# Kernel optimization log

Hardware: AMD Instinct MI355X
Metric: run time of the kernel (lower is better)

Reference implementation:

```python
import jax, jax.numpy as jnp
import numpy as np

D = 128       # embedding_dim
BC = 64       # block_count
BS = 512      # block_size
K = 6         # main conv kernel size
OV = 2 * BC   # overlap_size
SCALE = 1.0 / np.sqrt(D).astype(np.float32)


def setup_inputs() -> dict:
    key = jax.random.key(0)
    ks = jax.random.split(key, 6)
    B = 8
    x = jax.random.normal(ks[0], (B, BC * BS, D), dtype=jnp.float32)
    w_lw = jax.random.normal(ks[1], (D, 1), dtype=jnp.float32) * 0.05
    b_lw = jnp.zeros((1,), dtype=jnp.float32)
    conv_w = jax.random.normal(ks[2], (D, D, K), dtype=jnp.float32) * 0.05  # (out, in, k)
    conv_b = jnp.zeros((D,), dtype=jnp.float32)
    fusion_w = jax.random.normal(ks[3], (3 * D, D), dtype=jnp.float32) * 0.05
    fusion_b = jnp.zeros((D,), dtype=jnp.float32)
    return {"x": x, "w_lw": w_lw, "b_lw": b_lw, "conv_w": conv_w,
            "conv_b": conv_b, "fusion_w": fusion_w, "fusion_b": fusion_b}


def _prefix_softmax_weighted_sum(x, logits):
    # x: (B, L, D), logits: (B, L) -- faithful replica of the torch scan
    pmax = jax.lax.cummax(logits, axis=1)
    ex = jnp.exp(logits - pmax)                    # (B, L)
    psum = jnp.cumsum(ex, axis=1)                  # (B, L)
    wpre = jnp.cumsum(ex[..., None] * x, axis=1)   # (B, L, D)
    return wpre / psum[..., None]


def _attn(q, k, v):
    # q: (N, 1, D); k, v: (N, S, D)
    s = jnp.einsum('nqd,nkd->nqk', q, k) * SCALE
    return jnp.einsum('nqk,nkd->nqd', jax.nn.softmax(s, axis=-1), v)


def reference(x, w_lw, b_lw, conv_w, conv_b, fusion_w, fusion_b):
    B, L, _ = x.shape  # L == BC * BS, so F.pad in the original is a no-op
    logits = jax.nn.silu(x @ w_lw + b_lw)[..., 0]          # (B, L)
    prefix_x = _prefix_softmax_weighted_sum(x, logits) + x  # (B, L, D)

    # per-block conv1d (kernel 6, padding='same' in torch => pad (2,3))
    blocks = prefix_x.reshape(B * BC, BS, D).transpose(0, 2, 1)  # (N, D, BS)
    conv = jax.lax.conv_general_dilated(
        blocks, conv_w, window_strides=(1,), padding=[(2, 3)],
        dimension_numbers=('NCH', 'OIH', 'NCH')) + conv_b[None, :, None]
    blocks_c = conv.transpose(0, 2, 1)                           # (N, BS, D)
    block_repr = jnp.max(blocks_c, axis=1)[:, None, :]           # (N, 1, D)

    # overlap windows: replicate-pad end by OV//2, slice, gather OV-wide windows
    xov = jnp.pad(prefix_x, ((0, 0), (0, OV // 2), (0, 0)), mode='edge')
    xov = xov[:, BS - OV // 2:, :]                               # (B, (BC-1)*BS + OV, D)
    idx = (jnp.arange(BC) * BS)[:, None] + jnp.arange(OV)[None, :]  # (BC, OV)
    xbo = xov[:, idx, :].reshape(B * BC, OV, D)

    a_s = _attn(block_repr, blocks_c, blocks_c)  # block->self
    a_o = _attn(block_repr, xbo, xbo)            # block->overlap
    fused = jnp.concatenate([a_s, a_o, block_repr], axis=-1)    # (N, 1, 3D)
    out = (fused @ fusion_w + fusion_b).reshape(B, BC, D)
    return (out, out)
```

## Files before the change

kernel.cpp:

```cpp
#include <hip/hip_runtime.h>
#include <hip/hip_bf16.h>

#define NB 8
#define LSEQ 32768
#define DCH 128
#define NCHUNK 1024
#define NSUB 4096
#define NBLK 512
#define PH 520
#define SCALE_F 0.08838834764831845f

typedef __bf16 bf16x8 __attribute__((ext_vector_type(8)));
typedef float f32x4 __attribute__((ext_vector_type(4)));

__device__ __forceinline__ float bf2f(unsigned short u) {
    return __uint_as_float(((unsigned)u) << 16);
}
__device__ __forceinline__ unsigned short f2bf(float f) {
    unsigned u = __float_as_uint(f);
    u += 0x7fffu + ((u >> 16) & 1u);
    return (unsigned short)(u >> 16);
}

__device__ __forceinline__ void async_copy16(const void* gsrc, void* ldst) {
    __builtin_amdgcn_global_load_lds(
        (const __attribute__((address_space(1))) unsigned int*)gsrc,
        (__attribute__((address_space(3))) unsigned int*)ldst, 16, 0, 0);
}

__global__ __launch_bounds__(256) void k_logits2(const float* __restrict__ x,
                                                 const float* __restrict__ w_lw,
                                                 const float* __restrict__ b_lw,
                                                 float* __restrict__ logits,
                                                 float* __restrict__ subM) {
    int chunk = blockIdx.x, t = threadIdx.x;
    int g = t & 15, rs = t >> 4;
    __shared__ float sp[256 * 17];
    __shared__ float red[256];
    float wv[8];
    #pragma unroll
    for (int e = 0; e < 8; ++e) wv[e] = w_lw[g * 8 + e];
    float bb = b_lw[0];
    size_t base = (size_t)chunk * 256 * DCH;
    for (int i = 0; i < 16; ++i) {
        int row = rs * 16 + i;
        float4 a  = *(const float4*)(x + base + (size_t)row * DCH + g * 8);
        float4 b4 = *(const float4*)(x + base + (size_t)row * DCH + g * 8 + 4);
        sp[row * 17 + g] = a.x * wv[0] + a.y * wv[1] + a.z * wv[2] + a.w * wv[3] +
                           b4.x * wv[4] + b4.y * wv[5] + b4.z * wv[6] + b4.w * wv[7];
    }
    __syncthreads();
    float s = bb;
    #pragma unroll
    for (int j = 0; j < 16; ++j) s += sp[t * 17 + j];
    float l = s / (1.f + expf(-s));
    logits[(size_t)chunk * 256 + t] = l;
    red[t] = l;
    __syncthreads();
    for (int off = 32; off >= 1; off >>= 1) {
        if ((t & 63) < off) red[t] = fmaxf(red[t], red[t + off]);
        __syncthreads();
    }
    if ((t & 63) == 0) subM[chunk * 4 + (t >> 6)] = red[t];
}

__global__ __launch_bounds__(64) void k_seed_max2(const float* __restrict__ subM,
                                                  float* __restrict__ seedM) {
    int b = blockIdx.x, lane = threadIdx.x;
    const float* src = subM + b * 512;
    float* dst = seedM + b * 512;
    float v[8];
    float m = -INFINITY;
    #pragma unroll
    for (int j = 0; j < 8; ++j) { v[j] = src[lane * 8 + j]; m = fmaxf(m, v[j]); }
    float incl = m;
    #pragma unroll
    for (int off = 1; off < 64; off <<= 1) {
        float o = __shfl_up(incl, off, 64);
        if (lane >= off) incl = fmaxf(incl, o);
    }
    float ex = __shfl_up(incl, 1, 64);
    if (lane == 0) ex = -INFINITY;
    float run = ex;
    #pragma unroll
    for (int j = 0; j < 8; ++j) { dst[lane * 8 + j] = run; run = fmaxf(run, v[j]); }
}

__global__ __launch_bounds__(256) void k_sums(const float* __restrict__ x,
                                              const float* __restrict__ logits,
                                              const float* __restrict__ seedM,
                                              float* __restrict__ exg,
                                              float* __restrict__ S_w,
                                              float* __restrict__ S_wx) {
    int chunk = blockIdx.x, t = threadIdx.x;
    int g = t & 15, rs = t >> 4;
    __shared__ float llog[256];
    __shared__ float wbuf[256];
    __shared__ float red[256];
    __shared__ float rp[16 * 130];
    llog[t] = logits[(size_t)chunk * 256 + t];
    __syncthreads();
    if (t < 4) {
        float M = seedM[chunk * 4 + t];
        float m = -INFINITY;
        for (int i = 0; i < 64; ++i) {
            float l = llog[t * 64 + i];
            m = fmaxf(m, l);
            wbuf[t * 64 + i] = expf(l - fmaxf(M, m));
        }
    }
    __syncthreads();
    float w_t = wbuf[t];
    exg[(size_t)chunk * 256 + t] = w_t;
    red[t] = w_t;
    __syncthreads();
    for (int off = 32; off >= 1; off >>= 1) {
        if ((t & 63) < off) red[t] += red[t + off];
        __syncthreads();
    }
    if ((t & 63) == 0) S_w[chunk * 4 + (t >> 6)] = red[t];
    float acc[8];
    #pragma unroll
    for (int e = 0; e < 8; ++e) acc[e] = 0.f;
    size_t base = (size_t)chunk * 256 * DCH;
    for (int i = 0; i < 16; ++i) {
        int row = rs * 16 + i;
        float w = wbuf[row];
        float4 a  = *(const float4*)(x + base + (size_t)row * DCH + g * 8);
        float4 b4 = *(const float4*)(x + base + (size_t)row * DCH + g * 8 + 4);
        acc[0] += w * a.x;  acc[1] += w * a.y;  acc[2] += w * a.z;  acc[3] += w * a.w;
        acc[4] += w * b4.x; acc[5] += w * b4.y; acc[6] += w * b4.z; acc[7] += w * b4.w;
    }
    #pragma unroll
    for (int e = 0; e < 8; ++e) rp[rs * 130 + g * 8 + e] = acc[e];
    __syncthreads();
    #pragma unroll
    for (int k = 0; k < 2; ++k) {
        int idx = k * 256 + t;
        int sub = idx >> 7, c = idx & 127;
        float sm = rp[(sub * 4 + 0) * 130 + c] + rp[(sub * 4 + 1) * 130 + c] +
                   rp[(sub * 4 + 2) * 130 + c] + rp[(sub * 4 + 3) * 130 + c];
        S_wx[((size_t)chunk * 4 + sub) * DCH + c] = sm;
    }
}

__global__ __launch_bounds__(64) void k_seed_w(const float* __restrict__ S_w,
                                               float* __restrict__ sS_w) {
    int b = blockIdx.x, lane = threadIdx.x;
    const float* src = S_w + b * 512;
    float* dst = sS_w + b * 512;
    float v[8];
    float tot = 0.f;
    #pragma unroll
    for (int j = 0; j < 8; ++j) { v[j] = src[lane * 8 + j]; tot += v[j]; }
    float incl = tot;
    #pragma unroll
    for (int off = 1; off < 64; off <<= 1) {
        float o = __shfl_up(incl, off, 64);
        if (lane >= off) incl += o;
    }
    float ex = __shfl_up(incl, 1, 64);
    if (lane == 0) ex = 0.f;
    float run = ex;
    #pragma unroll
    for (int j = 0; j < 8; ++j) { dst[lane * 8 + j] = run; run += v[j]; }
}

__global__ __launch_bounds__(256) void k_seed_sums2(const float* __restrict__ S_wx,
                                                    float* __restrict__ sS_wx) {
    int b = blockIdx.x >> 3, cg = blockIdx.x & 7;
    int t = threadIdx.x;
    int cl = t & 15, seg = t >> 4;
    int c = cg * 16 + cl;
    __shared__ float tots[16][17];
    const float* src = S_wx + (size_t)b * 512 * DCH + c;
    float* dst = sS_wx + (size_t)b * 512 * DCH + c;
    int s0 = seg * 32;
    float tot = 0.f;
    for (int j = 0; j < 32; ++j) tot += src[(size_t)(s0 + j) * DCH];
    tots[seg][cl] = tot;
    __syncthreads();
    if (t < 16) {
        float run = 0.f;
        for (int s = 0; s < 16; ++s) { float tmp = tots[s][t]; tots[s][t] = run; run += tmp; }
    }
    __syncthreads();
    float run = tots[seg][cl];
    for (int j = 0; j < 32; ++j) {
        float val = src[(size_t)(s0 + j) * DCH];
        dst[(size_t)(s0 + j) * DCH] = run;
        run += val;
    }
}

__global__ __launch_bounds__(256) void k_zero_pad(unsigned short* __restrict__ P) {
    int n = blockIdx.x, t = threadIdx.x;
    for (int i = t; i < 1024; i += 256) {
        int rr = i >> 7;
        int row = (rr < 2) ? rr : 512 + rr;
        P[(n * PH + row) * DCH + (i & 127)] = 0;
    }
}

__global__ __launch_bounds__(128) void k_apply(const float* __restrict__ x,
                                               const float* __restrict__ exg,
                                               const float* __restrict__ sS_w,
                                               const float* __restrict__ sS_wx,
                                               unsigned short* __restrict__ P) {
    int t = threadIdx.x, w = t >> 6, lane = t & 63;
    int s = blockIdx.x * 2 + w;
    int b = s >> 9, sb = s & 511;
    __shared__ float e2[128];
    e2[t] = exg[(size_t)blockIdx.x * 128 + t];
    float2 axx = *(const float2*)(sS_wx + (size_t)s * DCH + 2 * lane);
    float aex = sS_w[s];
    __syncthreads();
    const float* es = e2 + w * 64;
    int pib0 = sb * 64;
    int n = b * 64 + (pib0 >> 9);
    int row0 = (pib0 & 511) + 2;
    const float* xp = x + ((size_t)b * LSEQ + pib0) * DCH + 2 * lane;
    unsigned short* pp = P + ((size_t)n * PH + row0) * DCH + 2 * lane;
    for (int j = 0; j < 64; ++j) {
        float e = es[j];
        aex += e;
        float2 xv = *(const float2*)xp;
        axx.x += e * xv.x;
        axx.y += e * xv.y;
        float inv = 1.f / aex;
        unsigned pk = ((unsigned)f2bf(axx.y * inv + xv.y) << 16) | f2bf(axx.x * inv + xv.x);
        *(unsigned*)pp = pk;
        xp += DCH;
        pp += DCH;
    }
}

__global__ __launch_bounds__(256) void k_w2t(const float* __restrict__ conv_w,
                                             unsigned short* __restrict__ W2t) {
    int idx = blockIdx.x * 256 + threadIdx.x;
    if (idx < 128 * 768) {
        int o = idx / 768, kk = idx % 768;
        int kn = kk >> 7, i = kk & 127;
        W2t[idx] = f2bf(conv_w[(o * 128 + i) * 6 + kn]);
    }
}

__global__ __launch_bounds__(256) void k_conv(const unsigned short* __restrict__ P,
                                              const unsigned short* __restrict__ W2t,
                                              const float* __restrict__ conv_b,
                                              unsigned short* __restrict__ convout) {
    int n = blockIdx.x >> 2;
    int h0 = (blockIdx.x & 3) * 128;
    __shared__ __align__(16) unsigned short lds[128 * 136];
    char* ldsA = (char*)lds;
    char* ldsB = (char*)lds + 16384;
    int t = threadIdx.x;
    int wave = t >> 6, lane = t & 63;
    f32x4 acc[4][4] = {};
    const unsigned short* Pn = P + (size_t)n * PH * DCH;
    int wm = (wave >> 1) * 64, wn = (wave & 1) * 64;
    int rdma = (lane >> 3);
    int cpos = lane & 7;

    for (int kt = 0; kt < 12; ++kt) {
        int kn = kt >> 1;
        int c0 = (kt & 1) * 64;
        __syncthreads();
        #pragma unroll
        for (int j = 0; j < 4; ++j) {
            int r = (wave * 4 + j) * 8 + rdma;
            int gr = h0 + kn + r;
            int csrcA = cpos ^ (gr & 7);
            async_copy16(Pn + (size_t)gr * DCH + c0 + csrcA * 8,
                         ldsA + (wave * 4 + j) * 1024 + lane * 16);
            int csrcB = cpos ^ (r & 7);
            async_copy16(W2t + (size_t)r * 768 + kt * 64 + csrcB * 8,
                         ldsB + (wave * 4 + j) * 1024 + lane * 16);
        }
        __syncthreads();
        #pragma unroll
        for (int ks = 0; ks < 2; ++ks) {
            bf16x8 af[4], bfr[4];
            #pragma unroll
            for (int mi = 0; mi < 4; ++mi) {
                int rA = wm + mi * 16 + (lane & 15);
                int pA = (ks * 4 + (lane >> 4)) ^ ((kn + rA) & 7);
                af[mi] = *(const bf16x8*)(ldsA + rA * 128 + pA * 16);
            }
            #pragma unroll
            for (int ni = 0; ni < 4; ++ni) {
                int oB = wn + ni * 16 + (lane & 15);
                int pB = (ks * 4 + (lane >> 4)) ^ (oB & 7);
                bfr[ni] = *(const bf16x8*)(ldsB + oB * 128 + pB * 16);
            }
            #pragma unroll
            for (int mi = 0; mi < 4; ++mi)
                #pragma unroll
                for (int ni = 0; ni < 4; ++ni)
                    acc[mi][ni] = __builtin_amdgcn_mfma_f32_16x16x32_bf16(af[mi], bfr[ni],
                                                                          acc[mi][ni], 0, 0, 0);
        }
    }
    __syncthreads();
    #pragma unroll
    for (int mi = 0; mi < 4; ++mi)
        #pragma unroll
        for (int ni = 0; ni < 4; ++ni) {
            int col = wn + ni * 16 + (lane & 15);
            float bias = conv_b[col];
            #pragma unroll
            for (int r = 0; r < 4; ++r) {
                int row = wm + mi * 16 + (lane >> 4) * 4 + r;
                lds[row * 136 + col] = f2bf(acc[mi][ni][r] + bias);
            }
        }
    __syncthreads();
    size_t base = (size_t)(n * 512 + h0) * DCH;
    #pragma unroll
    for (int it = 0; it < 8; ++it) {
        int idx = it * 256 + t;
        int row = idx >> 4, g = idx & 15;
        uint4 v = *(const uint4*)(lds + row * 136 + g * 8);
        *(uint4*)(convout + base + (size_t)row * DCH + g * 8) = v;
    }
}

__global__ __launch_bounds__(256) void k_as(const unsigned short* __restrict__ conv,
                                            float* __restrict__ block_repr,
                                            float* __restrict__ a_s) {
    int n = blockIdx.x, t = threadIdx.x;
    int g = t & 15, rs = t >> 4;
    __shared__ __align__(16) float sp[512 * 17];
    __shared__ float s[512];
    __shared__ float br[128];
    float* rp = sp;
    const unsigned short* base = conv + (size_t)n * 512 * DCH;

    float m[8];
    #pragma unroll
    for (int e = 0; e < 8; ++e) m[e] = -INFINITY;
    for (int i = 0; i < 32; ++i) {
        int row = i * 16 + rs;
        uint4 v = *(const uint4*)(base + row * DCH + g * 8);
        unsigned vv[4] = {v.x, v.y, v.z, v.w};
        #pragma unroll
        for (int e = 0; e < 4; ++e) {
            m[2 * e]     = fmaxf(m[2 * e],     bf2f((unsigned short)(vv[e] & 0xffff)));
            m[2 * e + 1] = fmaxf(m[2 * e + 1], bf2f((unsigned short)(vv[e] >> 16)));
        }
    }
    #pragma unroll
    for (int e = 0; e < 8; ++e) rp[rs * 130 + g * 8 + e] = m[e];
    __syncthreads();
    if (t < 128) {
        float bm = rp[t];
        #pragma unroll
        for (int r2 = 1; r2 < 16; ++r2) bm = fmaxf(bm, rp[r2 * 130 + t]);
        br[t] = bm;
        block_repr[n * DCH + t] = bm;
    }
    __syncthreads();

    float brv[8];
    #pragma unroll
    for (int e = 0; e < 8; ++e) brv[e] = br[g * 8 + e];
    for (int i = 0; i < 32; ++i) {
        int row = i * 16 + rs;
        uint4 v = *(const uint4*)(base + row * DCH + g * 8);
        unsigned vv[4] = {v.x, v.y, v.z, v.w};
        float p = 0.f;
        #pragma unroll
        for (int e = 0; e < 4; ++e) {
            p += bf2f((unsigned short)(vv[e] & 0xffff)) * brv[2 * e];
            p += bf2f((unsigned short)(vv[e] >> 16))    * brv[2 * e + 1];
        }
        sp[row * 17 + g] = p;
    }
    __syncthreads();
    #pragma unroll
    for (int rr = 0; rr < 2; ++rr) {
        int row = t * 2 + rr;
        float p = 0.f;
        #pragma unroll
        for (int j = 0; j < 16; ++j) p += sp[row * 17 + j];
        s[row] = p * SCALE_F;
    }
    __syncthreads();

    float* red = sp;
    float mm = fmaxf(s[t], s[t + 256]);
    __syncthreads();
    red[t] = mm;
    __syncthreads();
    for (int off = 128; off > 0; off >>= 1) {
        if (t < off) red[t] = fmaxf(red[t], red[t + off]);
        __syncthreads();
    }
    float smax = red[0];
    __syncthreads();
    float e0 = expf(s[t] - smax), e1 = expf(s[t + 256] - smax);
    red[t] = e0 + e1;
    __syncthreads();
    for (int off = 128; off > 0; off >>= 1) {
        if (t < off) red[t] += red[t + off];
        __syncthreads();
    }
    float inv = 1.f / red[0];
    __syncthreads();
    s[t] = e0 * inv;
    s[t + 256] = e1 * inv;
    __syncthreads();

    float acc[8];
    #pragma unroll
    for (int e = 0; e < 8; ++e) acc[e] = 0.f;
    for (int i = 0; i < 32; ++i) {
        int row = i * 16 + rs;
        float w = s[row];
        uint4 v = *(const uint4*)(base + row * DCH + g * 8);
        unsigned vv[4] = {v.x, v.y, v.z, v.w};
        #pragma unroll
        for (int e = 0; e < 4; ++e) {
            acc[2 * e]     += w * bf2f((unsigned short)(vv[e] & 0xffff));
            acc[2 * e + 1] += w * bf2f((unsigned short)(vv[e] >> 16));
        }
    }
    #pragma unroll
    for (int e = 0; e < 8; ++e) rp[rs * 130 + g * 8 + e] = acc[e];
    __syncthreads();
    if (t < 128) {
        float p = 0.f;
        #pragma unroll
        for (int r2 = 0; r2 < 16; ++r2) p += rp[r2 * 130 + t];
        a_s[n * DCH + t] = p;
    }
}

__global__ __launch_bounds__(256) void k_ao(const unsigned short* __restrict__ P,
                                            const float* __restrict__ block_repr,
                                            float* __restrict__ a_o) {
    int n = blockIdx.x, t = threadIdx.x;
    int g = t & 15, rs = t >> 4;
    int b = n >> 6, c = n & 63;
    __shared__ float br[128];
    __shared__ int rb[128];
    __shared__ __align__(16) float sp[128 * 17];
    __shared__ float s[128];
    __shared__ float red[128];
    if (t < 128) {
        br[t] = block_repr[n * DCH + t];
        int pib = (c + 1) * 512 - 64 + t;
        pib = min(pib, LSEQ - 1);
        int n2 = b * 64 + (pib >> 9);
        int row = (pib & 511) + 2;
        rb[t] = (n2 * PH + row) * DCH;
    }
    __syncthreads();
    float brv[8];
    #pragma unroll
    for (int e = 0; e < 8; ++e) brv[e] = br[g * 8 + e];
    #pragma unroll
    for (int r = 0; r < 8; ++r) {
        int row = rs * 8 + r;
        uint4 v = *(const uint4*)(P + rb[row] + g * 8);
        unsigned vv[4] = {v.x, v.y, v.z, v.w};
        float p = 0.f;
        #pragma unroll
        for (int e = 0; e < 4; ++e) {
            p += bf2f((unsigned short)(vv[e] & 0xffff)) * brv[2 * e];
            p += bf2f((unsigned short)(vv[e] >> 16))    * brv[2 * e + 1];
        }
        sp[row * 17 + g] = p;
    }
    __syncthreads();
    if (t < 128) {
        float p = 0.f;
        #pragma unroll
        for (int j = 0; j < 16; ++j) p += sp[t * 17 + j];
        s[t] = p * SCALE_F;
        red[t] = s[t];
    }
    __syncthreads();
    for (int off = 64; off > 0; off >>= 1) {
        if (t < off) red[t] = fmaxf(red[t], red[t + off]);
        __syncthreads();
    }
    float smax = red[0];
    __syncthreads();
    if (t < 128) {
        float e = expf(s[t] - smax);
        s[t] = e;
        red[t] = e;
    }
    __syncthreads();
    for (int off = 64; off > 0; off >>= 1) {
        if (t < off) red[t] += red[t + off];
        __syncthreads();
    }
    float inv = 1.f / red[0];
    __syncthreads();
    if (t < 128) s[t] *= inv;
    __syncthreads();
    float acc[8];
    #pragma unroll
    for (int e = 0; e < 8; ++e) acc[e] = 0.f;
    #pragma unroll
    for (int r = 0; r < 8; ++r) {
        int row = rs * 8 + r;
        float w = s[row];
        uint4 v = *(const uint4*)(P + rb[row] + g * 8);
        unsigned vv[4] = {v.x, v.y, v.z, v.w};
        #pragma unroll
        for (int e = 0; e < 4; ++e) {
            acc[2 * e]     += w * bf2f((unsigned short)(vv[e] & 0xffff));
            acc[2 * e + 1] += w * bf2f((unsigned short)(vv[e] >> 16));
        }
    }
    #pragma unroll
    for (int e = 0; e < 8; ++e) sp[rs * 130 + g * 8 + e] = acc[e];
    __syncthreads();
    if (t < 128) {
        float p = 0.f;
        #pragma unroll
        for (int r2 = 0; r2 < 16; ++r2) p += sp[r2 * 130 + t];
        a_o[n * DCH + t] = p;
    }
}

__global__ __launch_bounds__(128) void k_fusion(const float* __restrict__ a_s,
                                                const float* __restrict__ a_o,
                                                const float* __restrict__ block_repr,
                                                const float* __restrict__ fusion_w,
                                                const float* __restrict__ fusion_b,
                                                float* __restrict__ out) {
    int n = blockIdx.x, t = threadIdx.x;
    __shared__ float fu[384];
    fu[t] = a_s[n * DCH + t];
    fu[128 + t] = a_o[n * DCH + t];
    fu[256 + t] = block_repr[n * DCH + t];
    __syncthreads();
    float acc = fusion_b[t];
    for (int j = 0; j < 384; j++) acc += fu[j] * fusion_w[j * DCH + t];
    out[n * DCH + t] = acc;
    out[NB * 64 * DCH + n * DCH + t] = acc;
}

extern "C" void kernel_launch(void* const* d_in, const int* in_sizes, int n_in,
                              void* d_out, int out_size, void* d_ws, size_t ws_size,
                              hipStream_t stream) {
    const float* x        = (const float*)d_in[0];
    const float* w_lw     = (const float*)d_in[1];
    const float* b_lw     = (const float*)d_in[2];
    const float* conv_w   = (const float*)d_in[3];
    const float* conv_b   = (const float*)d_in[4];
    const float* fusion_w = (const float*)d_in[5];
    const float* fusion_b = (const float*)d_in[6];
    float* out = (float*)d_out;

    char* ws = (char*)d_ws;
    size_t off = 0;
    auto alloc = [&](size_t bytes) { char* p = ws + off; off += (bytes + 255) & ~(size_t)255; return p; };
    float* logits     = (float*)alloc(NB * LSEQ * 4);
    float* exg        = (float*)alloc(NB * LSEQ * 4);
    float* subM       = (float*)alloc(NSUB * 4);
    float* seedM      = (float*)alloc(NSUB * 4);
    float* S_w        = (float*)alloc(NSUB * 4);
    float* sS_w       = (float*)alloc(NSUB * 4);
    float* S_wx       = (float*)alloc((size_t)NSUB * DCH * 4);
    float* sS_wx      = (float*)alloc((size_t)NSUB * DCH * 4);
    float* block_repr = (float*)alloc(NBLK * DCH * 4);
    float* a_s        = (float*)alloc(NBLK * DCH * 4);
    float* a_o        = (float*)alloc(NBLK * DCH * 4);
    unsigned short* W2t     = (unsigned short*)alloc(128 * 768 * 2);
    unsigned short* P       = (unsigned short*)alloc((size_t)NBLK * PH * DCH * 2);
    unsigned short* convout = (unsigned short*)alloc((size_t)NBLK * 512 * DCH * 2);

    k_zero_pad<<<NBLK, 256, 0, stream>>>(P);
    k_w2t<<<384, 256, 0, stream>>>(conv_w, W2t);
    k_logits2<<<NCHUNK, 256, 0, stream>>>(x, w_lw, b_lw, logits, subM);
    k_seed_max2<<<NB, 64, 0, stream>>>(subM, seedM);
    k_sums<<<NCHUNK, 256, 0, stream>>>(x, logits, seedM, exg, S_w, S_wx);
    k_seed_w<<<NB, 64, 0, stream>>>(S_w, sS_w);
    k_seed_sums2<<<NB * 8, 256, 0, stream>>>(S_wx, sS_wx);
    k_apply<<<NSUB / 2, 128, 0, stream>>>(x, exg, sS_w, sS_wx, P);
    k_conv<<<NBLK * 4, 256, 0, stream>>>(P, W2t, conv_b, convout);
    k_as<<<NBLK, 256, 0, stream>>>(convout, block_repr, a_s);
    k_ao<<<NBLK, 256, 0, stream>>>(P, block_repr, a_o);
    k_fusion<<<NBLK, 128, 0, stream>>>(a_s, a_o, block_repr, fusion_w, fusion_b, out);
}
```

Baseline: 386.9 us.

## Double-buffer conv A tiles in LDS and load conv weights directly to registers

The conv GEMM kernel now double-buffers the activation tile in LDS, prefetching the next k-step while MFMAs run on the current one, and uses one barrier per iteration instead of two. Weights are re-laid out by the transpose kernel into an MFMA-fragment order, so each lane loads its B fragments straight from global memory into registers, also double-buffered, rather than staging them through LDS. This is meant to hide global load latency and cut LDS traffic. In exchange it raises register pressure (16 extra bf16x8 B fragments per lane plus the fully unrolled loop), which may reduce occupancy, and every block re-reads weights from L2.

```diff
diff --git a/kernel.cpp b/kernel.cpp
--- a/kernel.cpp
+++ b/kernel.cpp
@@ -236,72 +236,91 @@
 }
 
 __global__ __launch_bounds__(256) void k_w2t(const float* __restrict__ conv_w,
-                                             unsigned short* __restrict__ W2t) {
+                                             unsigned short* __restrict__ W3) {
     int idx = blockIdx.x * 256 + threadIdx.x;
-    if (idx < 128 * 768) {
-        int o = idx / 768, kk = idx % 768;
-        int kn = kk >> 7, i = kk & 127;
-        W2t[idx] = f2bf(conv_w[(o * 128 + i) * 6 + kn]);
+    if (idx < 98304) {
+        int e  = idx & 7;
+        int o  = (idx >> 3) & 127;
+        int kc = (idx >> 10) & 3;
+        int kt2 = idx >> 12;
+        int kt = kt2 >> 1, ks = kt2 & 1;
+        int i  = (kt & 1) * 64 + (ks * 4 + kc) * 8 + e;
+        int kn = kt >> 1;
+        W3[idx] = f2bf(conv_w[(o * 128 + i) * 6 + kn]);
     }
 }
 
 __global__ __launch_bounds__(256) void k_conv(const unsigned short* __restrict__ P,
-                                              const unsigned short* __restrict__ W2t,
+                                              const unsigned short* __restrict__ W3,
                                               const float* __restrict__ conv_b,
                                               unsigned short* __restrict__ convout) {
     int n = blockIdx.x >> 2;
     int h0 = (blockIdx.x & 3) * 128;
     __shared__ __align__(16) unsigned short lds[128 * 136];
-    char* ldsA = (char*)lds;
-    char* ldsB = (char*)lds + 16384;
+    char* abuf0 = (char*)lds;
+    char* abuf1 = (char*)lds + 16384;
     int t = threadIdx.x;
     int wave = t >> 6, lane = t & 63;
     f32x4 acc[4][4] = {};
     const unsigned short* Pn = P + (size_t)n * PH * DCH;
     int wm = (wave >> 1) * 64, wn = (wave & 1) * 64;
-    int rdma = (lane >> 3);
     int cpos = lane & 7;
-
-    for (int kt = 0; kt < 12; ++kt) {
-        int kn = kt >> 1;
-        int c0 = (kt & 1) * 64;
-        __syncthreads();
+    int kchunk = lane >> 4;
+    int bcol = wn + (lane & 15);
+
+    bf16x8 breg[2][8];
+
+    auto stageA = [&](int kt, char* dst) {
+        int kn = kt >> 1, c0 = (kt & 1) * 64;
         #pragma unroll
         for (int j = 0; j < 4; ++j) {
-            int r = (wave * 4 + j) * 8 + rdma;
+            int r = (wave * 4 + j) * 8 + (lane >> 3);
             int gr = h0 + kn + r;
             int csrcA = cpos ^ (gr & 7);
             async_copy16(Pn + (size_t)gr * DCH + c0 + csrcA * 8,
-                         ldsA + (wave * 4 + j) * 1024 + lane * 16);
-            int csrcB = cpos ^ (r & 7);
-            async_copy16(W2t + (size_t)r * 768 + kt * 64 + csrcB * 8,
-                         ldsB + (wave * 4 + j) * 1024 + lane * 16);
-        }
-        __syncthreads();
+                         dst + (wave * 4 + j) * 1024 + lane * 16);
+        }
+    };
+    auto loadB = [&](int kt, bf16x8* dstB) {
+        #pragma unroll
+        for (int ks = 0; ks < 2; ++ks)
+            #pragma unroll
+            for (int ni = 0; ni < 4; ++ni)
+                dstB[ks * 4 + ni] = *(const bf16x8*)(
+                    W3 + (size_t)((kt * 2 + ks) * 4 + kchunk) * 1024 + (bcol + ni * 16) * 8);
+    };
+
+    stageA(0, abuf0);
+    loadB(0, breg[0]);
+    __syncthreads();
+
+    #pragma unroll
+    for (int kt = 0; kt < 12; ++kt) {
+        char* cbuf = (kt & 1) ? abuf1 : abuf0;
+        if (kt < 11) {
+            stageA(kt + 1, (kt & 1) ? abuf0 : abuf1);
+            loadB(kt + 1, breg[(kt + 1) & 1]);
+        }
+        int kn = kt >> 1;
         #pragma unroll
         for (int ks = 0; ks < 2; ++ks) {
-            bf16x8 af[4], bfr[4];
+            bf16x8 af[4];
             #pragma unroll
             for (int mi = 0; mi < 4; ++mi) {
                 int rA = wm + mi * 16 + (lane & 15);
-                int pA = (ks * 4 + (lane >> 4)) ^ ((kn + rA) & 7);
-                af[mi] = *(const bf16x8*)(ldsA + rA * 128 + pA * 16);
-            }
-            #pragma unroll
-            for (int ni = 0; ni < 4; ++ni) {
-                int oB = wn + ni * 16 + (lane & 15);
-                int pB = (ks * 4 + (lane >> 4)) ^ (oB & 7);
-                bfr[ni] = *(const bf16x8*)(ldsB + oB * 128 + pB * 16);
+                int pA = (ks * 4 + kchunk) ^ ((kn + rA) & 7);
+                af[mi] = *(const bf16x8*)(cbuf + rA * 128 + pA * 16);
             }
             #pragma unroll
             for (int mi = 0; mi < 4; ++mi)
                 #pragma unroll
                 for (int ni = 0; ni < 4; ++ni)
-                    acc[mi][ni] = __builtin_amdgcn_mfma_f32_16x16x32_bf16(af[mi], bfr[ni],
+                    acc[mi][ni] = __builtin_amdgcn_mfma_f32_16x16x32_bf16(af[mi],
+                                                                          breg[kt & 1][ks * 4 + ni],
                                                                           acc[mi][ni], 0, 0, 0);
         }
-    }
-    __syncthreads();
+        __syncthreads();
+    }
     #pragma unroll
     for (int mi = 0; mi < 4; ++mi)
         #pragma unroll
@@ -571,19 +590,19 @@
     float* block_repr = (float*)alloc(NBLK * DCH * 4);
     float* a_s        = (float*)alloc(NBLK * DCH * 4);
     float* a_o        = (float*)alloc(NBLK * DCH * 4);
-    unsigned short* W2t     = (unsigned short*)alloc(128 * 768 * 2);
+    unsigned short* W3      = (unsigned short*)alloc(128 * 768 * 2);
     unsigned short* P       = (unsigned short*)alloc((size_t)NBLK * PH * DCH * 2);
     unsigned short* convout = (unsigned short*)alloc((size_t)NBLK * 512 * DCH * 2);
 
     k_zero_pad<<<NBLK, 256, 0, stream>>>(P);
-    k_w2t<<<384, 256, 0, stream>>>(conv_w, W2t);
+    k_w2t<<<384, 256, 0, stream>>>(conv_w, W3);
     k_logits2<<<NCHUNK, 256, 0, stream>>>(x, w_lw, b_lw, logits, subM);
     k_seed_max2<<<NB, 64, 0, stream>>>(subM, seedM);
     k_sums<<<NCHUNK, 256, 0, stream>>>(x, logits, seedM, exg, S_w, S_wx);
     k_seed_w<<<NB, 64, 0, stream>>>(S_w, sS_w);
     k_seed_sums2<<<NB * 8, 256, 0, stream>>>(S_wx, sS_wx);
     k_apply<<<NSUB / 2, 128, 0, stream>>>(x, exg, sS_w, sS_wx, P);
-    k_conv<<<NBLK * 4, 256, 0, stream>>>(P, W2t, conv_b, convout);
+    k_conv<<<NBLK * 4, 256, 0, stream>>>(P, W3, conv_b, convout);
     k_as<<<NBLK, 256, 0, stream>>>(convout, block_repr, a_s);
     k_ao<<<NBLK, 256, 0, stream>>>(P, block_repr, a_o);
     k_fusion<<<NBLK, 128, 0, stream>>>(a_s, a_o, block_repr, fusion_w, fusion_b, out);
```

New measurement: 377.0 us. 2.6% less time.
